# Kernel optimization log

Hardware: AMD Instinct MI355X
Metric: run time of the kernel (lower is better)

Reference implementation:

```python
import jax, jax.numpy as jnp
import numpy as np

SEQ, D, H, DH = 118, 128, 4, 32
NEG = -1e9


def _rope_tables():
    # matches the second (overwriting) computation in __init__: base=10000, dim=128
    ch = jnp.arange(0, D, 2, dtype=jnp.float32)
    inv_freq = 1.0 / (10000.0 ** (ch / D))
    t = jnp.arange(SEQ, dtype=jnp.float32)
    freqs = jnp.outer(t, inv_freq)                      # (118, 64)
    return jnp.cos(freqs).astype(jnp.bfloat16), jnp.sin(freqs).astype(jnp.bfloat16)


def _apply_rope(x, cos, sin):
    # x: (b, 118, 128); cos/sin: (118, 64) bf16 -> promote to f32 in the mul
    d = x.shape[-1] // 2
    x1, x2 = x[..., :d], x[..., d:]
    y1 = x1 * cos + x2 * sin
    y2 = -x1 * sin + x2 * cos
    return jnp.concatenate([y1, y2], axis=-1).astype(x.dtype)


def _layernorm(x, g, b, eps=1e-5):
    mu = jnp.mean(x, -1, keepdims=True)
    var = jnp.mean(jnp.square(x - mu), -1, keepdims=True)
    return (x - mu) * jax.lax.rsqrt(var + eps) * g + b


def _attention_block(x, qkv_w, qkv_b, fc2_w, fc2_b, cos, sin, mask):
    b = x.shape[0]
    qkv = x @ qkv_w.T + qkv_b                           # (b, 118, 384)
    q, k, v = jnp.split(qkv, 3, axis=-1)
    q = _apply_rope(q, cos, sin)
    k = _apply_rope(k, cos, sin)
    # faithful to view(b,118,32,4) + rearrange 'b l d h -> b h l d'
    to_heads = lambda t: jnp.transpose(t.reshape(b, SEQ, DH, H), (0, 3, 1, 2))
    q, k, v = to_heads(q), to_heads(k), to_heads(v)     # (b, 4, 118, 32)
    scores = jnp.einsum('bhqd,bhkd->bhqk', q, k) / jnp.sqrt(jnp.float32(DH))
    scores = jnp.where(mask, scores, NEG)
    attn = jax.nn.softmax(scores, axis=-1)
    y = jnp.einsum('bhqk,bhkd->bhqd', attn, v)          # (b, 4, 118, 32)
    y = jnp.transpose(y, (0, 2, 1, 3)).reshape(b, SEQ, D)
    return jax.nn.silu(y @ fc2_w.T + fc2_b)


def setup_inputs() -> dict:
    key = jax.random.key(0)
    ks = jax.random.split(key, 10)
    s = lambda fan_in: 1.0 / np.sqrt(fan_in)
    inp = {
        'x': jax.random.normal(ks[0], (8192, SEQ), jnp.float32),
        'fc1_w': jax.random.uniform(ks[1], (D, 1), jnp.float32, -1.0, 1.0),
        'fc1_b': jax.random.uniform(ks[2], (D,), jnp.float32, -1.0, 1.0),
        'qkv_w': jax.random.uniform(ks[3], (3 * D, D), jnp.float32, -s(D), s(D)),
        'qkv_b': jax.random.uniform(ks[4], (3 * D,), jnp.float32, -s(D), s(D)),
        'fc2_w': jax.random.uniform(ks[5], (D, D), jnp.float32, -s(D), s(D)),
        'fc2_b': jax.random.uniform(ks[6], (D,), jnp.float32, -s(D), s(D)),
        'fc3_w': jax.random.uniform(ks[7], (1, D), jnp.float32, -s(D), s(D)),
        'fc3_b': jax.random.uniform(ks[8], (1,), jnp.float32, -s(D), s(D)),
        'ln_g': jnp.ones((D,), jnp.float32),
        'ln_b': jnp.zeros((D,), jnp.float32),
    }
    return inp


def reference(x, fc1_w, fc1_b, qkv_w, qkv_b, fc2_w, fc2_b, fc3_w, fc3_b, ln_g, ln_b):
    cos, sin = _rope_tables()
    mask = jnp.tril(jnp.ones((SEQ, SEQ), dtype=bool))
    h = jax.nn.silu(x[..., None] @ fc1_w.T + fc1_b)     # (b, 118, 128)
    x1 = _attention_block(h, qkv_w, qkv_b, fc2_w, fc2_b, cos, sin, mask)
    x2 = x1 + _attention_block(_layernorm(x1, ln_g, ln_b), qkv_w, qkv_b, fc2_w, fc2_b, cos, sin, mask)
    return (x2 @ fc3_w.T + fc3_b).squeeze(-1)           # (b, 118)
```

## Files before the change

kernel.cpp:

```cpp
#include <hip/hip_runtime.h>
#include <hip/hip_bf16.h>

#define SEQ 118
#define YS  136
#define SQS 40
#define SVS 136

typedef __attribute__((ext_vector_type(8))) short short8;
typedef __attribute__((ext_vector_type(4))) float f32x4;

__device__ __forceinline__ f32x4 mfma16(short8 a, short8 b, f32x4 c){
  return __builtin_amdgcn_mfma_f32_16x16x32_bf16(a, b, c, 0, 0, 0);
}
__device__ __forceinline__ float bfr(float x){
  return __bfloat162float(__float2bfloat16(x));
}
__device__ __forceinline__ float rcpf(float x){ return __builtin_amdgcn_rcpf(x); }
__device__ __forceinline__ float fsilu(float z){
  return z * rcpf(1.f + exp2f(-1.442695041f * z));
}
__device__ __forceinline__ float rsum16(float v){
  v += __shfl_xor(v,1); v += __shfl_xor(v,2); v += __shfl_xor(v,4); v += __shfl_xor(v,8);
  return v;
}
__device__ __forceinline__ float rmax16(float v){
  v = fmaxf(v, __shfl_xor(v,1)); v = fmaxf(v, __shfl_xor(v,2));
  v = fmaxf(v, __shfl_xor(v,4)); v = fmaxf(v, __shfl_xor(v,8));
  return v;
}
__device__ __forceinline__ unsigned pack_bf2(float lo, float hi){
  __hip_bfloat162 h2 = __float22bfloat162_rn(float2{lo, hi});
  unsigned u; __builtin_memcpy(&u, &h2, 4);
  return u;
}

__global__ void prep_kernel(const float* __restrict__ qkv_w,
                            const float* __restrict__ fc2_w,
                            __hip_bfloat16* __restrict__ wbf){
  int i = blockIdx.x * 256 + threadIdx.x;
  int seg = i >> 14;
  int r   = i & 16383;
  int row = r >> 7;
  int k   = r & 127;
  float v;
  if (seg < 3){
    int h = row >> 5, n = row & 31;
    v = qkv_w[(seg*128 + 4*n + h)*128 + k];
  } else {
    int h = k >> 5, rr = k & 31;
    int dh = (rr >> 1) + (rr & 1)*16;
    v = fc2_w[row*128 + h*32 + dh];
  }
  wbf[i] = __float2bfloat16(v);
}

__launch_bounds__(512, 4)
__global__ void fused_kernel(const float* __restrict__ x,
                             const float* __restrict__ fc1_w, const float* __restrict__ fc1_b,
                             const float* __restrict__ qkv_b,
                             const float* __restrict__ fc2_b, const float* __restrict__ fc3_w,
                             const float* __restrict__ fc3_b,
                             const float* __restrict__ ln_g,  const float* __restrict__ ln_b,
                             const __hip_bfloat16* __restrict__ wbf,
                             float* __restrict__ out)
{
  __shared__ __align__(16) char smem[63328];
  __hip_bfloat16* Ybuf = (__hip_bfloat16*)(smem);
  __hip_bfloat16* sQP  = (__hip_bfloat16*)(smem + 32096);
  __hip_bfloat16* sK   = (__hip_bfloat16*)(smem + 42336);
  __hip_bfloat16* sVt  = (__hip_bfloat16*)(smem + 52576);
  float*          sCb  = (float*)        (smem + 61280);

  const __hip_bfloat16* wq  = wbf;
  const __hip_bfloat16* wk  = wbf + 16384;
  const __hip_bfloat16* wvw = wbf + 32768;
  const __hip_bfloat16* w2  = wbf + 49152;

  const int b    = blockIdx.x;
  const int tid  = threadIdx.x;
  const int wv   = tid >> 6;
  const int lane = tid & 63;
  const int c    = lane & 15;
  const int quad = lane >> 4;
  const int arow = wv*16 + c;

  {
    int i = tid;
    if (i < 512){
      float v;
      if      (i < 128) v = fc2_b[i];
      else if (i < 256) v = fc3_w[i-128];
      else if (i < 384) v = ln_g [i-256];
      else              v = ln_b [i-384];
      sCb[i] = v;
    }
  }
  __syncthreads();

  float o1[4];

  #pragma unroll 1
  for (int p = 0; p < 2; ++p){
    short8 afr[4];
    if (p == 0){
      float xs = (arow < SEQ) ? x[b*SEQ + arow] : 0.f;
      #pragma unroll
      for (int k4 = 0; k4 < 4; k4++){
        int d0 = k4*32 + quad*8;
        short8 fr;
        #pragma unroll
        for (int i = 0; i < 8; i++){
          float z = xs * fc1_w[d0+i] + fc1_b[d0+i];
          float v = fsilu(z);
          if (arow >= SEQ) v = 0.f;
          fr[i] = (short)__builtin_bit_cast(unsigned short, __float2bfloat16(v));
        }
        afr[k4] = fr;
      }
    } else {
      #pragma unroll
      for (int k4 = 0; k4 < 4; k4++){
        short8 fr = *(const short8*)(Ybuf + arow*YS + k4*32 + quad*8);
        if (arow >= SEQ) fr = (short8){0,0,0,0,0,0,0,0};
        afr[k4] = fr;
      }
    }

    #pragma unroll 1
    for (int h = 0; h < 4; ++h){
      const float invf = exp2f((float)(4*c + h) * (-0.20762050593045f));

      {
        const __hip_bfloat16* wpq = wq + (h*32 + c)*128 + quad*8;
        const __hip_bfloat16* wpk = wk + (h*32 + c)*128 + quad*8;
        f32x4 q0={0,0,0,0}, q1={0,0,0,0}, k0={0,0,0,0}, k1={0,0,0,0};
        #pragma unroll
        for (int k4 = 0; k4 < 4; k4++){
          short8 bq0 = *(const short8*)(wpq + k4*32);
          short8 bq1 = *(const short8*)(wpq + 2048 + k4*32);
          short8 bk0 = *(const short8*)(wpk + k4*32);
          short8 bk1 = *(const short8*)(wpk + 2048 + k4*32);
          q0 = mfma16(afr[k4], bq0, q0);
          q1 = mfma16(afr[k4], bq1, q1);
          k0 = mfma16(afr[k4], bk0, k0);
          k1 = mfma16(afr[k4], bk1, k1);
        }
        const float KSC = 0.25500526963f;
        float bQ0 = qkv_b[      4*c + h], bQ1 = qkv_b[ 64 + 4*c + h];
        float bK0 = qkv_b[128 + 4*c + h], bK1 = qkv_b[192 + 4*c + h];
        #pragma unroll
        for (int j = 0; j < 4; j++){
          int s = wv*16 + quad*4 + j;
          float ang = (float)s * invf;
          float cv = bfr(__cosf(ang)), sv = bfr(__sinf(ang));
          float cvq = cv*KSC, svq = sv*KSC;
          float xq1 = q0[j] + bQ0, xq2 = q1[j] + bQ1;
          float xk1 = k0[j] + bK0, xk2 = k1[j] + bK1;
          *(unsigned*)(sQP + s*SQS + 2*c) = pack_bf2( xq1*cvq + xq2*svq, -xq1*svq + xq2*cvq);
          *(unsigned*)(sK  + s*SQS + 2*c) = pack_bf2( xk1*cv  + xk2*sv , -xk1*sv  + xk2*cv );
        }
      }
      {
        const __hip_bfloat16* wpv = wvw + (h*32 + c)*128 + quad*8;
        f32x4 v0={0,0,0,0}, v1={0,0,0,0};
        #pragma unroll
        for (int k4 = 0; k4 < 4; k4++){
          short8 b0 = *(const short8*)(wpv + k4*32);
          short8 b1 = *(const short8*)(wpv + 2048 + k4*32);
          v0 = mfma16(afr[k4], b0, v0);
          v1 = mfma16(afr[k4], b1, v1);
        }
        float bV0 = qkv_b[256 + 4*c + h], bV1 = qkv_b[320 + 4*c + h];
        int s0 = wv*16 + quad*4;
        *(unsigned*)(sVt + (c   )*SVS + s0    ) = pack_bf2(v0[0]+bV0, v0[1]+bV0);
        *(unsigned*)(sVt + (c   )*SVS + s0 + 2) = pack_bf2(v0[2]+bV0, v0[3]+bV0);
        *(unsigned*)(sVt + (c+16)*SVS + s0    ) = pack_bf2(v1[0]+bV1, v1[1]+bV1);
        *(unsigned*)(sVt + (c+16)*SVS + s0 + 2) = pack_bf2(v1[2]+bV1, v1[3]+bV1);
      }
      __syncthreads();

      short8 aq = *(const short8*)(sQP + arow*SQS + quad*8);
      f32x4 sc[8];
      #pragma unroll
      for (int t = 0; t < 8; t++){
        sc[t] = (f32x4){0.f,0.f,0.f,0.f};
        if (t <= wv){
          short8 bk = *(const short8*)(sK + (t*16 + c)*SQS + quad*8);
          f32x4 z = {0,0,0,0};
          sc[t] = mfma16(aq, bk, z);
        }
      }
      float rnorm[4];
      #pragma unroll
      for (int j = 0; j < 4; j++){
        float mx = -3.0e38f;
        #pragma unroll
        for (int t = 0; t < 8; t++){
          if (t < wv){
            mx = fmaxf(mx, sc[t][j]);
          } else if (t == wv){
            float v = (c <= quad*4 + j) ? sc[t][j] : -1.0e9f;
            sc[t][j] = v;
            mx = fmaxf(mx, v);
          }
        }
        mx = rmax16(mx);
        float sum = 0.f;
        #pragma unroll
        for (int t = 0; t < 8; t++) if (t <= wv){
          float e = exp2f(sc[t][j] - mx); sc[t][j] = e; sum += e;
        }
        sum = rsum16(sum);
        rnorm[j] = rcpf(sum);
      }

      f32x4 y0 = {0,0,0,0}, y1 = {0,0,0,0};
      auto pv_quarter = [&](int qt, f32x4 pa, f32x4 pb){
        int s0 = wv*16 + quad*4;
        #pragma unroll
        for (int j = 0; j < 4; j++){
          sQP[(s0+j)*SQS + c     ] = __float2bfloat16(pa[j]);
          sQP[(s0+j)*SQS + 16 + c] = __float2bfloat16(pb[j]);
        }
        short8 ap  = *(const short8*)(sQP + arow*SQS + quad*8);
        short8 bv0 = *(const short8*)(sVt + (c   )*SVS + qt*32 + quad*8);
        short8 bv1 = *(const short8*)(sVt + (c+16)*SVS + qt*32 + quad*8);
        y0 = mfma16(ap, bv0, y0);
        y1 = mfma16(ap, bv1, y1);
      };
      int qmax = wv >> 1;
      pv_quarter(0, sc[0], sc[1]);
      if (qmax >= 1) pv_quarter(1, sc[2], sc[3]);
      if (qmax >= 2) pv_quarter(2, sc[4], sc[5]);
      if (qmax >= 3) pv_quarter(3, sc[6], sc[7]);
      #pragma unroll
      for (int j = 0; j < 4; j++){ y0[j] *= rnorm[j]; y1[j] *= rnorm[j]; }

      {
        int s0 = wv*16 + quad*4;
        #pragma unroll
        for (int j = 0; j < 4; j++)
          if (s0 + j < SEQ)
            *(unsigned*)(Ybuf + (s0+j)*YS + h*32 + 2*c) = pack_bf2(y0[j], y1[j]);
      }
      __syncthreads();
    }

    short8 ay[4];
    #pragma unroll
    for (int k4 = 0; k4 < 4; k4++)
      ay[k4] = *(const short8*)(Ybuf + arow*YS + k4*32 + quad*8);
    f32x4 xx[8];
    f32x4 S1 = {0,0,0,0}, S2 = {0,0,0,0}, S3 = {0,0,0,0};
    #pragma unroll 1
    for (int t = 0; t < 8; t++){
      f32x4 acc = {0,0,0,0};
      #pragma unroll
      for (int k4 = 0; k4 < 4; k4++){
        short8 bw = *(const short8*)(w2 + (t*16 + c)*128 + k4*32 + quad*8);
        acc = mfma16(ay[k4], bw, acc);
      }
      float bias = sCb[t*16 + c];
      float w3   = sCb[128 + t*16 + c];
      #pragma unroll
      for (int j = 0; j < 4; j++){
        float v = fsilu(acc[j] + bias);
        xx[t][j] = v;
        S1[j] += v; S2[j] += v*v; S3[j] += v*w3;
      }
    }
    #pragma unroll
    for (int j = 0; j < 4; j++){
      float s1 = rsum16(S1[j]), s2 = rsum16(S2[j]), s3 = rsum16(S3[j]);
      int s = wv*16 + quad*4 + j;
      if (p == 0){
        float mu  = s1 * (1.f/128.f);
        float var = fmaxf(s2 * (1.f/128.f) - mu*mu, 0.f);
        float rs  = rsqrtf(var + 1e-5f);
        if (s < SEQ){
          #pragma unroll
          for (int t = 0; t < 8; t++){
            int d = t*16 + c;
            Ybuf[s*YS + d] = __float2bfloat16((xx[t][j] - mu)*rs*sCb[256+d] + sCb[384+d]);
          }
        }
        o1[j] = s3;
      } else {
        if (c == 0 && s < SEQ) out[b*SEQ + s] = o1[j] + s3 + fc3_b[0];
      }
    }
    if (p == 0) __syncthreads();
  }
}

extern "C" void kernel_launch(void* const* d_in, const int* in_sizes, int n_in,
                              void* d_out, int out_size, void* d_ws, size_t ws_size,
                              hipStream_t stream){
  const float* x     = (const float*)d_in[0];
  const float* fc1_w = (const float*)d_in[1];
  const float* fc1_b = (const float*)d_in[2];
  const float* qkv_w = (const float*)d_in[3];
  const float* qkv_b = (const float*)d_in[4];
  const float* fc2_w = (const float*)d_in[5];
  const float* fc2_b = (const float*)d_in[6];
  const float* fc3_w = (const float*)d_in[7];
  const float* fc3_b = (const float*)d_in[8];
  const float* ln_g  = (const float*)d_in[9];
  const float* ln_b  = (const float*)d_in[10];

  __hip_bfloat16* wbf = (__hip_bfloat16*)d_ws;
  prep_kernel<<<256, 256, 0, stream>>>(qkv_w, fc2_w, wbf);

  const int B = in_sizes[0] / SEQ;
  fused_kernel<<<B, 512, 0, stream>>>(x, fc1_w, fc1_b, qkv_b, fc2_b, fc3_w, fc3_b,
                                      ln_g, ln_b, wbf, (float*)d_out);
}
```

Before: 2.531 ms.

## Alias Ybuf with attention scratch in LDS and keep per-head outputs in registers

Overlaps the Y buffer with the Q/K/V attention scratch region, shrinking shared memory from about 63KB to 36KB and raising the launch-bounds occupancy hint from 4 to 6. Per-head attention outputs are held as packed bf16 in registers until every head is done, then written to Ybuf, with the head loop fully unrolled. Probabilities are packed to bf16 once before the PV stage, and the barriers move to match the new aliasing. The goal is more resident blocks per CU, at the cost of register pressure that the tighter launch bound may turn into spills.

Result: slower. 6.940 ms (+174.2%).

```diff
diff --git a/kernel.cpp b/kernel.cpp
--- a/kernel.cpp
+++ b/kernel.cpp
@@ -8,6 +8,7 @@
 
 typedef __attribute__((ext_vector_type(8))) short short8;
 typedef __attribute__((ext_vector_type(4))) float f32x4;
+typedef __attribute__((ext_vector_type(4))) unsigned u32x4;
 
 __device__ __forceinline__ f32x4 mfma16(short8 a, short8 b, f32x4 c){
   return __builtin_amdgcn_mfma_f32_16x16x32_bf16(a, b, c, 0, 0, 0);
@@ -54,7 +55,7 @@
   wbf[i] = __float2bfloat16(v);
 }
 
-__launch_bounds__(512, 4)
+__launch_bounds__(512, 6)
 __global__ void fused_kernel(const float* __restrict__ x,
                              const float* __restrict__ fc1_w, const float* __restrict__ fc1_b,
                              const float* __restrict__ qkv_b,
@@ -64,12 +65,12 @@
                              const __hip_bfloat16* __restrict__ wbf,
                              float* __restrict__ out)
 {
-  __shared__ __align__(16) char smem[63328];
+  __shared__ __align__(16) char smem[36864];
+  __hip_bfloat16* sQP  = (__hip_bfloat16*)(smem);
+  __hip_bfloat16* sK   = (__hip_bfloat16*)(smem + 10240);
+  __hip_bfloat16* sVt  = (__hip_bfloat16*)(smem + 20480);
   __hip_bfloat16* Ybuf = (__hip_bfloat16*)(smem);
-  __hip_bfloat16* sQP  = (__hip_bfloat16*)(smem + 32096);
-  __hip_bfloat16* sK   = (__hip_bfloat16*)(smem + 42336);
-  __hip_bfloat16* sVt  = (__hip_bfloat16*)(smem + 52576);
-  float*          sCb  = (float*)        (smem + 61280);
+  float*          sCb  = (float*)        (smem + 34816);
 
   const __hip_bfloat16* wq  = wbf;
   const __hip_bfloat16* wk  = wbf + 16384;
@@ -124,9 +125,12 @@
         if (arow >= SEQ) fr = (short8){0,0,0,0,0,0,0,0};
         afr[k4] = fr;
       }
-    }
-
-    #pragma unroll 1
+      __syncthreads();
+    }
+
+    unsigned ypk[4][4];
+
+    #pragma unroll
     for (int h = 0; h < 4; ++h){
       const float invf = exp2f((float)(4*c + h) * (-0.20762050593045f));
 
@@ -214,13 +218,23 @@
         rnorm[j] = rcpf(sum);
       }
 
+      u32x4 pp0, pp1, pp2, pp3;
+      #pragma unroll
+      for (int j = 0; j < 4; j++){
+        pp0[j] = pack_bf2(sc[0][j], sc[1][j]);
+        pp1[j] = pack_bf2(sc[2][j], sc[3][j]);
+        pp2[j] = pack_bf2(sc[4][j], sc[5][j]);
+        pp3[j] = pack_bf2(sc[6][j], sc[7][j]);
+      }
+
       f32x4 y0 = {0,0,0,0}, y1 = {0,0,0,0};
-      auto pv_quarter = [&](int qt, f32x4 pa, f32x4 pb){
+      auto pv_quarter = [&](int qt, u32x4 pq){
         int s0 = wv*16 + quad*4;
         #pragma unroll
         for (int j = 0; j < 4; j++){
-          sQP[(s0+j)*SQS + c     ] = __float2bfloat16(pa[j]);
-          sQP[(s0+j)*SQS + 16 + c] = __float2bfloat16(pb[j]);
+          unsigned u = pq[j];
+          *(unsigned short*)(sQP + (s0+j)*SQS + c     ) = (unsigned short)(u & 0xffffu);
+          *(unsigned short*)(sQP + (s0+j)*SQS + 16 + c) = (unsigned short)(u >> 16);
         }
         short8 ap  = *(const short8*)(sQP + arow*SQS + quad*8);
         short8 bv0 = *(const short8*)(sVt + (c   )*SVS + qt*32 + quad*8);
@@ -229,21 +243,27 @@
         y1 = mfma16(ap, bv1, y1);
       };
       int qmax = wv >> 1;
-      pv_quarter(0, sc[0], sc[1]);
-      if (qmax >= 1) pv_quarter(1, sc[2], sc[3]);
-      if (qmax >= 2) pv_quarter(2, sc[4], sc[5]);
-      if (qmax >= 3) pv_quarter(3, sc[6], sc[7]);
-      #pragma unroll
-      for (int j = 0; j < 4; j++){ y0[j] *= rnorm[j]; y1[j] *= rnorm[j]; }
-
-      {
-        int s0 = wv*16 + quad*4;
+      pv_quarter(0, pp0);
+      if (qmax >= 1) pv_quarter(1, pp1);
+      if (qmax >= 2) pv_quarter(2, pp2);
+      if (qmax >= 3) pv_quarter(3, pp3);
+
+      #pragma unroll
+      for (int j = 0; j < 4; j++)
+        ypk[h][j] = pack_bf2(y0[j]*rnorm[j], y1[j]*rnorm[j]);
+
+      __syncthreads();
+    }
+
+    {
+      int s0 = wv*16 + quad*4;
+      #pragma unroll
+      for (int h = 0; h < 4; ++h){
         #pragma unroll
         for (int j = 0; j < 4; j++)
           if (s0 + j < SEQ)
-            *(unsigned*)(Ybuf + (s0+j)*YS + h*32 + 2*c) = pack_bf2(y0[j], y1[j]);
-      }
-      __syncthreads();
+            *(unsigned*)(Ybuf + (s0+j)*YS + h*32 + 2*c) = ypk[h][j];
+      }
     }
 
     short8 ay[4];
@@ -289,7 +309,6 @@
         if (c == 0 && s < SEQ) out[b*SEQ + s] = o1[j] + s3 + fc3_b[0];
       }
     }
-    if (p == 0) __syncthreads();
   }
 }
 
```
